# Kernel tuning notes

Hardware: AMD Instinct MI355X
Metric: run time of the kernel (lower is better)

Reference implementation:

```python
import jax, jax.numpy as jnp
import numpy as np

S, NB, C = 7, 2, 20
LAMBDA_COORD, LAMBDA_NOOBJ = 5.0, 0.5
EPS = 1e-6


def _iou(a, b):
    """Midpoint-format IoU. a, b: [..., 4] = (x, y, w, h)."""
    ax1, ay1 = a[..., 0] - a[..., 2] / 2, a[..., 1] - a[..., 3] / 2
    ax2, ay2 = a[..., 0] + a[..., 2] / 2, a[..., 1] + a[..., 3] / 2
    bx1, by1 = b[..., 0] - b[..., 2] / 2, b[..., 1] - b[..., 3] / 2
    bx2, by2 = b[..., 0] + b[..., 2] / 2, b[..., 1] + b[..., 3] / 2
    iw = jnp.clip(jnp.minimum(ax2, bx2) - jnp.maximum(ax1, bx1), 0.0)
    ih = jnp.clip(jnp.minimum(ay2, by2) - jnp.maximum(ay1, by1), 0.0)
    inter = iw * ih
    area_a = jnp.abs((ax2 - ax1) * (ay2 - ay1))
    area_b = jnp.abs((bx2 - bx1) * (by2 - by1))
    return inter / (area_a + area_b - inter + EPS)


def setup_inputs() -> dict:
    key = jax.random.key(0)
    k1, k2, k3, k4 = jax.random.split(key, 4)
    N = 16384
    predictions = jax.random.uniform(k1, (N, S * S * (C + NB * 5)), dtype=jnp.float32)
    cls = jax.random.uniform(k2, (N, S, S, C), dtype=jnp.float32)
    box_rest = jax.random.uniform(k3, (N, S, S, 4), dtype=jnp.float32)  # y,w,h,conf
    u = jax.random.uniform(k4, (N, S, S, 2), dtype=jnp.float32)
    flag = jnp.where(u[..., 0] < 0.3, 1.0, u[..., 1] * 0.99)
    targets = jnp.concatenate([cls, flag[..., None], box_rest], axis=-1)  # [N,S,S,25]
    return {"predictions": predictions, "targets": targets}


def reference(predictions, targets):
    N = predictions.shape[0]
    pred = predictions.reshape(N, S, S, C + NB * 5)
    class_pred = pred[..., :C]                      # [N,S,S,20]
    b1 = pred[..., C:C + 5]                         # [N,S,S,5]
    b2 = pred[..., C + 5:C + 10]                    # [N,S,S,5]
    tbox = targets[..., C:C + 5]                    # [N,S,S,5]
    obj = (targets[..., C] == 1.0).astype(pred.dtype)  # [N,S,S]

    iou1 = _iou(b1[..., :4], tbox[..., :4])
    iou2 = _iou(b2[..., :4], tbox[..., :4])
    resp = jnp.where((iou1 > iou2)[..., None], b1, b2)  # responsible box [N,S,S,5]

    xy = (resp[..., 0] - tbox[..., 0]) ** 2 + (resp[..., 1] - tbox[..., 1]) ** 2
    wh = (jnp.sqrt(resp[..., 2]) - jnp.sqrt(tbox[..., 2])) ** 2 \
       + (jnp.sqrt(resp[..., 3]) - jnp.sqrt(tbox[..., 3])) ** 2
    coord = LAMBDA_COORD * (xy + wh)
    conf = (resp[..., 4] - tbox[..., 4]) ** 2
    cls_loss = jnp.sum((class_pred - targets[..., :C]) ** 2, axis=-1)

    obj_terms = jnp.sum(obj * (coord + conf + cls_loss))
    noobj_terms = LAMBDA_NOOBJ * jnp.sum((1.0 - obj) * (b1[..., 4] ** 2 + b2[..., 4] ** 2))
    return (obj_terms + noobj_terms) / N
```

## Files before the change

kernel.cpp:

```cpp
#include <hip/hip_runtime.h>
#include <math.h>

#define SS 7
#define CC 20
#define CELL_PRED 30
#define CELL_TGT  25
#define BLOCK 256
#define GRID 1024

__device__ __forceinline__ float cell_loss(const float* __restrict__ pred,
                                           const float* __restrict__ tgt,
                                           int c) {
    const float EPS = 1e-6f;
    const float* tp = tgt + (size_t)c * CELL_TGT;
    float tv[CELL_TGT];
    #pragma unroll
    for (int j = 0; j < CELL_TGT; ++j) tv[j] = tp[j];

    const float2* p2 = (const float2*)(pred + (size_t)c * CELL_PRED);
    float cls = 0.0f;
    #pragma unroll
    for (int j = 0; j < 10; ++j) {
        float2 v = p2[j];
        float d0 = v.x - tv[2 * j];
        float d1 = v.y - tv[2 * j + 1];
        cls += d0 * d0;
        cls += d1 * d1;
    }
    float b[10];
    #pragma unroll
    for (int j = 0; j < 5; ++j) {
        float2 v = p2[10 + j];
        b[2 * j] = v.x; b[2 * j + 1] = v.y;
    }
    const float* b1 = b;
    const float* b2 = b + 5;
    const float* tb = tv + CC;

    float obj = (tb[0] == 1.0f) ? 1.0f : 0.0f;

    float t_x1 = tb[0] - tb[2] * 0.5f, t_y1 = tb[1] - tb[3] * 0.5f;
    float t_x2 = tb[0] + tb[2] * 0.5f, t_y2 = tb[1] + tb[3] * 0.5f;
    float t_area = fabsf((t_x2 - t_x1) * (t_y2 - t_y1));

    float a_x1 = b1[0] - b1[2] * 0.5f, a_y1 = b1[1] - b1[3] * 0.5f;
    float a_x2 = b1[0] + b1[2] * 0.5f, a_y2 = b1[1] + b1[3] * 0.5f;
    float iw1 = fmaxf(fminf(a_x2, t_x2) - fmaxf(a_x1, t_x1), 0.0f);
    float ih1 = fmaxf(fminf(a_y2, t_y2) - fmaxf(a_y1, t_y1), 0.0f);
    float inter1 = iw1 * ih1;
    float area1 = fabsf((a_x2 - a_x1) * (a_y2 - a_y1));
    float iou1 = inter1 / (area1 + t_area - inter1 + EPS);

    float c_x1 = b2[0] - b2[2] * 0.5f, c_y1 = b2[1] - b2[3] * 0.5f;
    float c_x2 = b2[0] + b2[2] * 0.5f, c_y2 = b2[1] + b2[3] * 0.5f;
    float iw2 = fmaxf(fminf(c_x2, t_x2) - fmaxf(c_x1, t_x1), 0.0f);
    float ih2 = fmaxf(fminf(c_y2, t_y2) - fmaxf(c_y1, t_y1), 0.0f);
    float inter2 = iw2 * ih2;
    float area2 = fabsf((c_x2 - c_x1) * (c_y2 - c_y1));
    float iou2 = inter2 / (area2 + t_area - inter2 + EPS);

    bool pick1 = iou1 > iou2;
    float r0 = pick1 ? b1[0] : b2[0];
    float r1 = pick1 ? b1[1] : b2[1];
    float r2 = pick1 ? b1[2] : b2[2];
    float r3 = pick1 ? b1[3] : b2[3];
    float r4 = pick1 ? b1[4] : b2[4];

    float dx = r0 - tb[0], dy = r1 - tb[1];
    float xy = dx * dx + dy * dy;
    float dw = sqrtf(r2) - sqrtf(tb[2]);
    float dh = sqrtf(r3) - sqrtf(tb[3]);
    float wh = dw * dw + dh * dh;
    float coord = 5.0f * (xy + wh);
    float dconf = r4 - tb[4];
    float conf = dconf * dconf;

    float noobj = 0.5f * (1.0f - obj) * (b1[4] * b1[4] + b2[4] * b2[4]);
    return obj * (coord + conf + cls) + noobj;
}

__global__ __launch_bounds__(BLOCK) void yolo_stream(
    const float* __restrict__ pred,
    const float* __restrict__ tgt,
    float* __restrict__ partials,
    int nCells, int fullIters)
{
    const int tid = threadIdx.x;
    int c = blockIdx.x * BLOCK + tid;
    const int stride = GRID * BLOCK;

    float loss = 0.0f;
    for (int it = 0; it < fullIters; ++it, c += stride)
        loss += cell_loss(pred, tgt, c);
    if (c < nCells)
        loss += cell_loss(pred, tgt, c);

    #pragma unroll
    for (int off = 32; off > 0; off >>= 1)
        loss += __shfl_down(loss, off, 64);
    __shared__ float s_red[4];
    if ((tid & 63) == 0) s_red[tid >> 6] = loss;
    __syncthreads();
    if (tid == 0)
        partials[blockIdx.x] = (s_red[0] + s_red[1]) + (s_red[2] + s_red[3]);
}

__global__ __launch_bounds__(BLOCK) void yolo_final_reduce(
    const float* __restrict__ partials, int nPartials, double invN,
    float* __restrict__ out)
{
    __shared__ double s_red[4];
    const float4* p4 = (const float4*)partials;
    double sum = 0.0;
    for (int i = threadIdx.x; i < (nPartials >> 2); i += BLOCK) {
        float4 v = p4[i];
        sum += (double)v.x + (double)v.y + (double)v.z + (double)v.w;
    }
    for (int i = ((nPartials >> 2) << 2) + threadIdx.x; i < nPartials; i += BLOCK)
        sum += (double)partials[i];
    #pragma unroll
    for (int off = 32; off > 0; off >>= 1)
        sum += __shfl_down(sum, off, 64);
    if ((threadIdx.x & 63) == 0) s_red[threadIdx.x >> 6] = sum;
    __syncthreads();
    if (threadIdx.x == 0) {
        double s = (s_red[0] + s_red[1]) + (s_red[2] + s_red[3]);
        out[0] = (float)(s * invN);
    }
}

extern "C" void kernel_launch(void* const* d_in, const int* in_sizes, int n_in,
                              void* d_out, int out_size, void* d_ws, size_t ws_size,
                              hipStream_t stream) {
    const float* pred = (const float*)d_in[0];
    const float* tgt  = (const float*)d_in[1];
    float* out = (float*)d_out;
    float* partials = (float*)d_ws;

    const int N = in_sizes[0] / (SS * SS * CELL_PRED);
    const int nCells = N * SS * SS;
    const int stride = GRID * BLOCK;
    const int fullIters = nCells / stride;

    yolo_stream<<<GRID, BLOCK, 0, stream>>>(pred, tgt, partials, nCells, fullIters);
    yolo_final_reduce<<<1, BLOCK, 0, stream>>>(partials, GRID, 1.0 / (double)N, out);
}
```

Baseline: 197.2 us.

## Stage cell tiles into LDS via async global_load_lds with double buffering

Each 64-thread block now copies contiguous 64-cell tiles of predictions and targets into LDS using global_load_lds, double-buffered so the next tile loads while the current one is computed. Threads then read their cell from LDS, replacing strided per-thread global loads with fully coalesced 16-byte transfers. This adds manual vmcnt waits and an LDS footprint of about 28 KB per block, and it shrinks blocks to a single wave, which may limit occupancy and latency hiding.

```diff
diff --git a/kernel.cpp b/kernel.cpp
--- a/kernel.cpp
+++ b/kernel.cpp
@@ -5,19 +5,46 @@
 #define CC 20
 #define CELL_PRED 30
 #define CELL_TGT  25
-#define BLOCK 256
 #define GRID 1024
+#define TPB 64
+#define REDUCE_BLOCK 256
 
-__device__ __forceinline__ float cell_loss(const float* __restrict__ pred,
+
+#define PRED_TILE_B 7680
+#define TGT_TILE_B  6400
+#define TILE_FLOATS 3520
+
+__device__ __forceinline__ void stage_tile(const float* __restrict__ pred,
                                            const float* __restrict__ tgt,
-                                           int c) {
+                                           size_t t, float* lbuf, int lane)
+{
+    const char* gp = (const char*)pred + t * (size_t)PRED_TILE_B;
+    const char* gt = (const char*)tgt  + t * (size_t)TGT_TILE_B;
+    char* lp = (char*)lbuf;
+    #pragma unroll
+    for (int k = 0; k < 7; ++k)
+        __builtin_amdgcn_global_load_lds((const float*)(gp + k * 1024 + lane * 16),
+                                         (float*)(lp + k * 1024), 16, 0, 0);
+    #pragma unroll
+    for (int k = 0; k < 2; ++k)
+        __builtin_amdgcn_global_load_lds((const float*)(gp + 7168 + k * 256 + lane * 4),
+                                         (float*)(lp + 7168 + k * 256), 4, 0, 0);
+    #pragma unroll
+    for (int k = 0; k < 6; ++k)
+        __builtin_amdgcn_global_load_lds((const float*)(gt + k * 1024 + lane * 16),
+                                         (float*)(lp + PRED_TILE_B + k * 1024), 16, 0, 0);
+    __builtin_amdgcn_global_load_lds((const float*)(gt + 6144 + lane * 4),
+                                     (float*)(lp + PRED_TILE_B + 6144), 4, 0, 0);
+}
+
+__device__ __forceinline__ float cell_loss_ptr(const float* __restrict__ pc,
+                                               const float* __restrict__ tc) {
     const float EPS = 1e-6f;
-    const float* tp = tgt + (size_t)c * CELL_TGT;
     float tv[CELL_TGT];
     #pragma unroll
-    for (int j = 0; j < CELL_TGT; ++j) tv[j] = tp[j];
+    for (int j = 0; j < CELL_TGT; ++j) tv[j] = tc[j];
 
-    const float2* p2 = (const float2*)(pred + (size_t)c * CELL_PRED);
+    const float2* p2 = (const float2*)pc;
     float cls = 0.0f;
     #pragma unroll
     for (int j = 0; j < 10; ++j) {
@@ -79,44 +106,64 @@
     return obj * (coord + conf + cls) + noobj;
 }
 
-__global__ __launch_bounds__(BLOCK) void yolo_stream(
+__global__ __launch_bounds__(TPB) void yolo_stream(
     const float* __restrict__ pred,
     const float* __restrict__ tgt,
     float* __restrict__ partials,
-    int nCells, int fullIters)
+    int nCells)
 {
-    const int tid = threadIdx.x;
-    int c = blockIdx.x * BLOCK + tid;
-    const int stride = GRID * BLOCK;
+    __shared__ __align__(16) float lds[2][TILE_FLOATS];
+    const int lane = threadIdx.x;
+    const int bid  = blockIdx.x;
+    const int nTiles = nCells >> 6;
 
     float loss = 0.0f;
-    for (int it = 0; it < fullIters; ++it, c += stride)
-        loss += cell_loss(pred, tgt, c);
-    if (c < nCells)
-        loss += cell_loss(pred, tgt, c);
+    const int myT = (bid < nTiles) ? ((nTiles - bid - 1) / GRID + 1) : 0;
+
+    if (myT > 0) {
+        float* bufA = lds[0];
+        float* bufB = lds[1];
+        size_t t = (size_t)bid;
+        stage_tile(pred, tgt, t, bufA, lane);
+        for (int i = 0; i < myT; ++i) {
+            asm volatile("" ::: "memory");
+            if (i + 1 < myT) {
+                stage_tile(pred, tgt, t + GRID, bufB, lane);
+                asm volatile("s_waitcnt vmcnt(16)" ::: "memory");
+            } else {
+                asm volatile("s_waitcnt vmcnt(0)" ::: "memory");
+            }
+            loss += cell_loss_ptr(bufA + lane * CELL_PRED,
+                                  bufA + (PRED_TILE_B / 4) + lane * CELL_TGT);
+            float* tmp = bufA; bufA = bufB; bufB = tmp;
+            t += GRID;
+        }
+    }
+
+    if (bid == 0) {
+        for (int c = (nTiles << 6) + lane; c < nCells; c += TPB)
+            loss += cell_loss_ptr(pred + (size_t)c * CELL_PRED,
+                                  tgt  + (size_t)c * CELL_TGT);
+    }
 
     #pragma unroll
     for (int off = 32; off > 0; off >>= 1)
         loss += __shfl_down(loss, off, 64);
-    __shared__ float s_red[4];
-    if ((tid & 63) == 0) s_red[tid >> 6] = loss;
-    __syncthreads();
-    if (tid == 0)
-        partials[blockIdx.x] = (s_red[0] + s_red[1]) + (s_red[2] + s_red[3]);
+    if (lane == 0) partials[bid] = loss;
 }
 
-__global__ __launch_bounds__(BLOCK) void yolo_final_reduce(
+__global__ __launch_bounds__(REDUCE_BLOCK) void yolo_final_reduce(
     const float* __restrict__ partials, int nPartials, double invN,
     float* __restrict__ out)
 {
     __shared__ double s_red[4];
     const float4* p4 = (const float4*)partials;
     double sum = 0.0;
-    for (int i = threadIdx.x; i < (nPartials >> 2); i += BLOCK) {
+    for (int i = threadIdx.x; i < (nPartials >> 2); i += REDUCE_BLOCK) {
         float4 v = p4[i];
         sum += (double)v.x + (double)v.y + (double)v.z + (double)v.w;
     }
-    for (int i = ((nPartials >> 2) << 2) + threadIdx.x; i < nPartials; i += BLOCK)
+    for (int i = ((nPartials >> 2) << 2) + threadIdx.x; i < nPartials; i += REDUCE_BLOCK)
         sum += (double)partials[i];
     #pragma unroll
     for (int off = 32; off > 0; off >>= 1)
@@ -139,9 +186,7 @@
 
     const int N = in_sizes[0] / (SS * SS * CELL_PRED);
     const int nCells = N * SS * SS;
-    const int stride = GRID * BLOCK;
-    const int fullIters = nCells / stride;
 
-    yolo_stream<<<GRID, BLOCK, 0, stream>>>(pred, tgt, partials, nCells, fullIters);
-    yolo_final_reduce<<<1, BLOCK, 0, stream>>>(partials, GRID, 1.0 / (double)N, out);
+    yolo_stream<<<GRID, TPB, 0, stream>>>(pred, tgt, partials, nCells);
+    yolo_final_reduce<<<1, REDUCE_BLOCK, 0, stream>>>(partials, GRID, 1.0 / (double)N, out);
 }
```

Measured after the change: 193.3 us. No clear change (-2.0%).

## Process cells in quads with 16-byte aligned float4 loads and wave-tiled scheduling

Applied to the files above, without the earlier changes.

Each thread now handles four consecutive cells, so that prediction (120 floats) and target (100 floats) quads start on 16-byte boundaries. All loads become float4 instead of float2 and scalar loads, with template offsets selecting the right sub-range. Work is split into 64-quad tiles assigned per wave with a strided schedule, plus a tail path handled by one wave. This is meant to cut memory instruction count and improve load efficiency, at the cost of more registers per thread (occupancy is hinted with launch_bounds 3) and some redundant loaded elements.

```diff
diff --git a/kernel.cpp b/kernel.cpp
--- a/kernel.cpp
+++ b/kernel.cpp
@@ -5,37 +5,24 @@
 #define CC 20
 #define CELL_PRED 30
 #define CELL_TGT  25
-#define BLOCK 256
+#define TPB 256
+#define WAVES 4
 #define GRID 1024
+#define NSTREAM (GRID * WAVES)
+#define REDUCE_BLOCK 256
 
-__device__ __forceinline__ float cell_loss(const float* __restrict__ pred,
-                                           const float* __restrict__ tgt,
-                                           int c) {
+
+__device__ __forceinline__ float cell_math(const float* pv, const float* tv) {
     const float EPS = 1e-6f;
-    const float* tp = tgt + (size_t)c * CELL_TGT;
-    float tv[CELL_TGT];
-    #pragma unroll
-    for (int j = 0; j < CELL_TGT; ++j) tv[j] = tp[j];
-
-    const float2* p2 = (const float2*)(pred + (size_t)c * CELL_PRED);
     float cls = 0.0f;
     #pragma unroll
-    for (int j = 0; j < 10; ++j) {
-        float2 v = p2[j];
-        float d0 = v.x - tv[2 * j];
-        float d1 = v.y - tv[2 * j + 1];
-        cls += d0 * d0;
-        cls += d1 * d1;
+    for (int k = 0; k < CC; ++k) {
+        float d = pv[k] - tv[k];
+        cls += d * d;
     }
-    float b[10];
-    #pragma unroll
-    for (int j = 0; j < 5; ++j) {
-        float2 v = p2[10 + j];
-        b[2 * j] = v.x; b[2 * j + 1] = v.y;
-    }
-    const float* b1 = b;
-    const float* b2 = b + 5;
-    const float* tb = tv + CC;
+    const float* b1 = pv + 20;
+    const float* b2 = pv + 25;
+    const float* tb = tv + 20;
 
     float obj = (tb[0] == 1.0f) ? 1.0f : 0.0f;
 
@@ -79,44 +66,93 @@
     return obj * (coord + conf + cls) + noobj;
 }
 
-__global__ __launch_bounds__(BLOCK) void yolo_stream(
+template<int PO, int TO>
+__device__ __forceinline__ float cell_from_f4(const float4* __restrict__ gp,
+                                              const float4* __restrict__ gt) {
+    float pv[32], tv[28];
+    #pragma unroll
+    for (int k = 0; k < 8; ++k) {
+        float4 a = gp[k];
+        pv[4 * k] = a.x; pv[4 * k + 1] = a.y; pv[4 * k + 2] = a.z; pv[4 * k + 3] = a.w;
+    }
+    #pragma unroll
+    for (int k = 0; k < 7; ++k) {
+        float4 a = gt[k];
+        tv[4 * k] = a.x; tv[4 * k + 1] = a.y; tv[4 * k + 2] = a.z; tv[4 * k + 3] = a.w;
+    }
+    return cell_math(pv + PO, tv + TO);
+}
+
+__device__ __forceinline__ float quad_loss(const float4* __restrict__ gp,
+                                           const float4* __restrict__ gt) {
+    float s = 0.0f;
+    s += cell_from_f4<0, 0>(gp,      gt);
+    s += cell_from_f4<2, 1>(gp + 7,  gt + 6);
+    s += cell_from_f4<0, 2>(gp + 15, gt + 12);
+    s += cell_from_f4<2, 3>(gp + 22, gt + 18);
+    return s;
+}
+
+__global__ __launch_bounds__(TPB, 3) void yolo_stream(
     const float* __restrict__ pred,
     const float* __restrict__ tgt,
     float* __restrict__ partials,
-    int nCells, int fullIters)
+    int nCells)
 {
-    const int tid = threadIdx.x;
-    int c = blockIdx.x * BLOCK + tid;
-    const int stride = GRID * BLOCK;
+    __shared__ float s_red[WAVES];
+    const int tid  = threadIdx.x;
+    const int lane = tid & 63;
+    const int wid  = tid >> 6;
+    const int b    = blockIdx.x;
 
+    const int nQuads = nCells >> 2;
+    const int nTiles = nQuads >> 6;
+
+    const int k = ((b >> 8) << 2) + wid;
     float loss = 0.0f;
-    for (int it = 0; it < fullIters; ++it, c += stride)
-        loss += cell_loss(pred, tgt, c);
-    if (c < nCells)
-        loss += cell_loss(pred, tgt, c);
+
+    const float4* predF4 = (const float4*)pred;
+    const float4* tgtF4  = (const float4*)tgt;
+
+    for (int tile = (b & 255) + (k << 8); tile < nTiles; tile += NSTREAM) {
+        int q = (tile << 6) + lane;
+        loss += quad_loss(predF4 + (size_t)q * 30, tgtF4 + (size_t)q * 25);
+    }
+
+    if (b == 0 && wid == 0) {
+        for (int q = (nTiles << 6) + lane; q < nQuads; q += 64)
+            loss += quad_loss(predF4 + (size_t)q * 30, tgtF4 + (size_t)q * 25);
+        for (int c = (nQuads << 2) + lane; c < nCells; c += 64) {
+            float pv[CELL_PRED], tv[CELL_TGT];
+            #pragma unroll
+            for (int j = 0; j < CELL_PRED; ++j) pv[j] = pred[(size_t)c * CELL_PRED + j];
+            #pragma unroll
+            for (int j = 0; j < CELL_TGT; ++j)  tv[j] = tgt[(size_t)c * CELL_TGT + j];
+            loss += cell_math(pv, tv);
+        }
+    }
 
     #pragma unroll
     for (int off = 32; off > 0; off >>= 1)
         loss += __shfl_down(loss, off, 64);
-    __shared__ float s_red[4];
-    if ((tid & 63) == 0) s_red[tid >> 6] = loss;
+    if (lane == 0) s_red[wid] = loss;
     __syncthreads();
     if (tid == 0)
-        partials[blockIdx.x] = (s_red[0] + s_red[1]) + (s_red[2] + s_red[3]);
+        partials[b] = (s_red[0] + s_red[1]) + (s_red[2] + s_red[3]);
 }
 
-__global__ __launch_bounds__(BLOCK) void yolo_final_reduce(
+__global__ __launch_bounds__(REDUCE_BLOCK) void yolo_final_reduce(
     const float* __restrict__ partials, int nPartials, double invN,
     float* __restrict__ out)
 {
     __shared__ double s_red[4];
     const float4* p4 = (const float4*)partials;
     double sum = 0.0;
-    for (int i = threadIdx.x; i < (nPartials >> 2); i += BLOCK) {
+    for (int i = threadIdx.x; i < (nPartials >> 2); i += REDUCE_BLOCK) {
         float4 v = p4[i];
         sum += (double)v.x + (double)v.y + (double)v.z + (double)v.w;
     }
-    for (int i = ((nPartials >> 2) << 2) + threadIdx.x; i < nPartials; i += BLOCK)
+    for (int i = ((nPartials >> 2) << 2) + threadIdx.x; i < nPartials; i += REDUCE_BLOCK)
         sum += (double)partials[i];
     #pragma unroll
     for (int off = 32; off > 0; off >>= 1)
@@ -139,9 +175,7 @@
 
     const int N = in_sizes[0] / (SS * SS * CELL_PRED);
     const int nCells = N * SS * SS;
-    const int stride = GRID * BLOCK;
-    const int fullIters = nCells / stride;
 
-    yolo_stream<<<GRID, BLOCK, 0, stream>>>(pred, tgt, partials, nCells, fullIters);
-    yolo_final_reduce<<<1, BLOCK, 0, stream>>>(partials, GRID, 1.0 / (double)N, out);
+    yolo_stream<<<GRID, TPB, 0, stream>>>(pred, tgt, partials, nCells);
+    yolo_final_reduce<<<1, REDUCE_BLOCK, 0, stream>>>(partials, GRID, 1.0 / (double)N, out);
 }
```

New measurement: 205.3 us. +4.1%, slower.
